# Performance work log

Hardware: AMD Instinct MI355X
Metric: run time of the kernel (lower is better)

The kernel has to match this reference:

```python
import jax, jax.numpy as jnp
import numpy as np

BATCH, NUM_M, NUM_USER, FEAT_B = 512, 64, 32, 62
CH = [64, 512, 512, 512]  # digital_channel; input = 2 (D feat) + 62 (B_norm feat)


def setup_inputs() -> dict:
    key = jax.random.key(0)
    ks = jax.random.split(key, 12)
    D = jax.random.normal(ks[0], (BATCH, NUM_USER, 2), dtype=jnp.float32)
    B = jax.random.uniform(ks[1], (BATCH, NUM_M, NUM_USER, FEAT_B), dtype=jnp.float32)
    P_pow_normalized = jnp.float32(1.0)
    D_0 = jax.random.normal(ks[2], (BATCH, NUM_USER, 2), dtype=jnp.float32)
    # MLP params: Lin(64,512)+ReLU, Lin(512,512)+ReLU, Lin(512,512)+ReLU, Lin(512,2)+Sigmoid
    def lin(k, fin, fout):
        bound = 1.0 / np.sqrt(fin)
        kw, kb = jax.random.split(k)
        W = jax.random.uniform(kw, (fin, fout), dtype=jnp.float32, minval=-bound, maxval=bound)
        b = jax.random.uniform(kb, (fout,), dtype=jnp.float32, minval=-bound, maxval=bound)
        return W, b
    W1, b1 = lin(ks[3], CH[0], CH[1])
    W2, b2 = lin(ks[4], CH[1], CH[2])
    W3, b3 = lin(ks[5], CH[2], CH[3])
    W4, b4 = lin(ks[6], CH[3], 2)
    return {"D": D, "B": B, "P_pow_normalized": P_pow_normalized, "D_0": D_0,
            "W1": W1, "b1": b1, "W2": W2, "b2": b2,
            "W3": W3, "b3": b3, "W4": W4, "b4": b4}


def reference(D, B, P_pow_normalized, D_0, W1, b1, W2, b2, W3, b3, W4, b4):
    # aggregate analog-side messages over antennas (dim 1): [batch, num_user, feat_B]
    B_norm = jnp.sum(B, axis=1)
    # per-user gather + concat -> [batch, num_user, ch0]
    x = jnp.concatenate([D, B_norm], axis=-1)
    # MLP applied row-wise (row ordering in the torch loop is irrelevant to the math)
    h = jax.nn.relu(x @ W1 + b1)
    h = jax.nn.relu(h @ W2 + b2)
    h = jax.nn.relu(h @ W3 + b3)
    D_1 = jax.nn.sigmoid(h @ W4 + b4)  # [batch, num_user, 2]
    # per-batch normalize over users, scale by power budget
    D_sum = jnp.sum(D_1, axis=1, keepdims=True)  # [batch, 1, 2]
    return P_pow_normalized * (D_1 / D_sum)
```

## Files before the change

### kernel.cpp

```cpp
#include <hip/hip_runtime.h>
#include <hip/hip_bf16.h>
#include <cstdint>
#include <cstddef>

#define BATCH 512
#define NUSER 32
#define NM    64
#define FEATB 62

typedef short bf16x8 __attribute__((ext_vector_type(8)));
typedef float f32x4  __attribute__((ext_vector_type(4)));
typedef float f32x4v __attribute__((ext_vector_type(4)));

__device__ __forceinline__ float bf2f(short s) {
    union { unsigned int u; float f; } v;
    v.u = ((unsigned int)(unsigned short)s) << 16;
    return v.f;
}

__global__ void transpose_cvt_all_kernel(
        const float* __restrict__ W1, const float* __restrict__ W2,
        const float* __restrict__ W3, const float* __restrict__ W4,
        __hip_bfloat16* __restrict__ WT1, __hip_bfloat16* __restrict__ WT2,
        __hip_bfloat16* __restrict__ WT3, __hip_bfloat16* __restrict__ WT4) {
    __shared__ float t[64][65];
    const int idx = blockIdx.x;
    const float* W; __hip_bfloat16* WT; int K, N, kt, nt;
    if (idx < 8)        { W = W1; WT = WT1; K = 64;  N = 512; kt = 0;             nt = idx;          }
    else if (idx < 72)  { W = W2; WT = WT2; K = 512; N = 512; kt = (idx-8) >> 3;  nt = (idx-8) & 7;  }
    else if (idx < 136) { W = W3; WT = WT3; K = 512; N = 512; kt = (idx-72) >> 3; nt = (idx-72) & 7; }
    else                { W = W4; WT = WT4; K = 512; N = 2;   kt = idx - 136;     nt = 0;            }
    const int k0 = kt * 64, n0 = nt * 64;
    #pragma unroll
    for (int i = 0; i < 16; ++i) {
        int lin = threadIdx.x + i * 256;
        int r = lin >> 6, c = lin & 63;
        if (k0 + r < K && n0 + c < N) t[r][c] = W[(size_t)(k0 + r) * N + (n0 + c)];
    }
    __syncthreads();
    #pragma unroll
    for (int i = 0; i < 16; ++i) {
        int lin = threadIdx.x + i * 256;
        int r = lin >> 6, c = lin & 63;
        if (n0 + r < N && k0 + c < K)
            WT[(size_t)(n0 + r) * K + (k0 + c)] = __float2bfloat16(t[c][r]);
    }
}

__device__ __forceinline__ void xs_store_pair(char* xs, int row, int col, float a, float b) {
    __hip_bfloat162 h;
    h.x = __float2bfloat16(a); h.y = __float2bfloat16(b);
    *reinterpret_cast<__hip_bfloat162*>(
        xs + (((unsigned)row * 128u + (unsigned)col * 2u) ^ ((unsigned)(row & 7) << 4))) = h;
}
__device__ __forceinline__ void xs_store4(char* xs, int j, float s0, float s1, float s2, float s3) {
    const int e = 4 * j;
    const int user = e / FEATB, feat = e % FEATB;
    xs_store_pair(xs, user, 2 + feat, s0, s1);
    if (feat == 60) xs_store_pair(xs, user + 1, 2, s2, s3);
    else            xs_store_pair(xs, user, 4 + feat, s2, s3);
}

template<int K, int ASTRIDE>
__device__ __forceinline__ void mlp_layer(const char* a_lds,
                                          const __hip_bfloat16* __restrict__ wt,
                                          const float* __restrict__ bias,
                                          char* out_lds,
                                          int wave, int lane) {
    f32x4 acc[2][8] = {};
    const int colbase = wave * 128;
    const int lrow = lane & 15;
    const int kg   = (lane >> 4) * 8;
    const unsigned int sw = (unsigned int)(lrow & 7) << 4;

    #pragma unroll 2
    for (int ks = 0; ks < K / 32; ++ks) {
        const int k0 = ks * 32 + kg;
        bf16x8 a0 = *reinterpret_cast<const bf16x8*>(a_lds + ((((unsigned)lrow        * ASTRIDE + k0 * 2)) ^ sw));
        bf16x8 a1 = *reinterpret_cast<const bf16x8*>(a_lds + ((((unsigned)(16 + lrow) * ASTRIDE + k0 * 2)) ^ sw));
        bf16x8 bfrag[8];
        #pragma unroll
        for (int n = 0; n < 8; ++n) {
            const int col = colbase + n * 16 + lrow;
            bfrag[n] = *reinterpret_cast<const bf16x8*>(wt + (size_t)col * K + k0);
        }
        #pragma unroll
        for (int n = 0; n < 8; ++n) {
            acc[0][n] = __builtin_amdgcn_mfma_f32_16x16x32_bf16(a0, bfrag[n], acc[0][n], 0, 0, 0);
            acc[1][n] = __builtin_amdgcn_mfma_f32_16x16x32_bf16(a1, bfrag[n], acc[1][n], 0, 0, 0);
        }
    }

    const int rg = (lane >> 4) * 4;
    #pragma unroll
    for (int m = 0; m < 2; ++m) {
        #pragma unroll
        for (int n = 0; n < 8; ++n) {
            const int col = colbase + n * 16 + lrow;
            const float bv = bias[col];
            #pragma unroll
            for (int r = 0; r < 4; ++r) {
                const int row = m * 16 + rg + r;
                float v = acc[m][n][r] + bv;
                v = fmaxf(v, 0.f);
                *reinterpret_cast<__hip_bfloat16*>(
                    out_lds + (((unsigned)row * 1024u + (unsigned)col * 2u) ^ ((unsigned)(row & 7) << 4)))
                    = __float2bfloat16(v);
            }
        }
    }
}

__global__ __launch_bounds__(256, 2) void fused_kernel(
    const float* __restrict__ B, const float* __restrict__ D,
    const __hip_bfloat16* __restrict__ WT1, const float* __restrict__ b1,
    const __hip_bfloat16* __restrict__ WT2, const float* __restrict__ b2,
    const __hip_bfloat16* __restrict__ WT3, const float* __restrict__ b3,
    const __hip_bfloat16* __restrict__ WT4, const float* __restrict__ b4,
    const float* __restrict__ Pp, float* __restrict__ out) {

    __shared__ __align__(16) char xs[NUSER * 64 * 2];
    __shared__ __align__(16) char act0[NUSER * 512 * 2];
    __shared__ __align__(16) char act1[NUSER * 512 * 2];
    __shared__ float d1s[NUSER][2];
    __shared__ float colsum[2];

    const int batch = blockIdx.x;
    const int tid = threadIdx.x;
    const int wave = tid >> 6, lane = tid & 63;

    {
        const f32x4v* p = reinterpret_cast<const f32x4v*>(B + (size_t)batch * (NM * NUSER * FEATB));
        const int j0 = tid, j1 = tid + 256;
        const bool hasj1 = (j1 < 496);
        f32x4v s0 = {0.f, 0.f, 0.f, 0.f};
        f32x4v s1 = {0.f, 0.f, 0.f, 0.f};
        #pragma unroll 4
        for (int m = 0; m < NM; ++m) {
            s0 += __builtin_nontemporal_load(p + (size_t)j0 + (size_t)m * 496);
            if (hasj1)
                s1 += __builtin_nontemporal_load(p + (size_t)j1 + (size_t)m * 496);
        }
        xs_store4(xs, j0, s0.x, s0.y, s0.z, s0.w);
        if (hasj1) {
            xs_store4(xs, j1, s1.x, s1.y, s1.z, s1.w);
        } else {
            const int dj = tid - 240;
            float4 v = reinterpret_cast<const float4*>(D + (size_t)batch * NUSER * 2)[dj];
            xs_store_pair(xs, 2 * dj,     0, v.x, v.y);
            xs_store_pair(xs, 2 * dj + 1, 0, v.z, v.w);
        }
    }
    __syncthreads();

    mlp_layer<64, 128>(xs, WT1, b1, act0, wave, lane);
    __syncthreads();
    mlp_layer<512, 1024>(act0, WT2, b2, act1, wave, lane);
    __syncthreads();
    mlp_layer<512, 1024>(act1, WT3, b3, act0, wave, lane);
    __syncthreads();

    {
        const int row = tid >> 3, col = (tid >> 2) & 1, part = tid & 3;
        float s = 0.f;
        #pragma unroll
        for (int kk = 0; kk < 128; kk += 8) {
            const int k = part * 128 + kk;
            bf16x8 av = *reinterpret_cast<const bf16x8*>(
                act0 + (((unsigned)row * 1024u + (unsigned)k * 2u) ^ ((unsigned)(row & 7) << 4)));
            bf16x8 wv = *reinterpret_cast<const bf16x8*>(WT4 + col * 512 + k);
            #pragma unroll
            for (int jj = 0; jj < 8; ++jj) s += bf2f(av[jj]) * bf2f(wv[jj]);
        }
        s += __shfl_xor(s, 1, 64);
        s += __shfl_xor(s, 2, 64);
        if (part == 0) {
            const float z = s + b4[col];
            d1s[row][col] = 1.f / (1.f + expf(-z));
        }
    }
    __syncthreads();

    if (tid < 2) {
        float s = 0.f;
        #pragma unroll
        for (int r = 0; r < NUSER; ++r) s += d1s[r][tid];
        colsum[tid] = s;
    }
    __syncthreads();
    if (tid < 64) {
        out[(size_t)batch * 64 + tid] = Pp[0] * d1s[tid >> 1][tid & 1] / colsum[tid & 1];
    }
}

extern "C" void kernel_launch(void* const* d_in, const int* in_sizes, int n_in,
                              void* d_out, int out_size, void* d_ws, size_t ws_size,
                              hipStream_t stream) {
    const float* D  = (const float*)d_in[0];
    const float* B  = (const float*)d_in[1];
    const float* Pp = (const float*)d_in[2];
    const float* W1 = (const float*)d_in[4];
    const float* b1 = (const float*)d_in[5];
    const float* W2 = (const float*)d_in[6];
    const float* b2 = (const float*)d_in[7];
    const float* W3 = (const float*)d_in[8];
    const float* b3 = (const float*)d_in[9];
    const float* W4 = (const float*)d_in[10];
    const float* b4 = (const float*)d_in[11];
    float* out = (float*)d_out;

    char* ws = (char*)d_ws;
    __hip_bfloat16* WT1 = (__hip_bfloat16*)(ws);
    __hip_bfloat16* WT2 = (__hip_bfloat16*)(ws + 65536);
    __hip_bfloat16* WT3 = (__hip_bfloat16*)(ws + 65536 + 524288);
    __hip_bfloat16* WT4 = (__hip_bfloat16*)(ws + 65536 + 524288 + 524288);

    transpose_cvt_all_kernel<<<144, 256, 0, stream>>>(W1, W2, W3, W4, WT1, WT2, WT3, WT4);

    fused_kernel<<<BATCH, 256, 0, stream>>>(B, D, WT1, b1, WT2, b2, WT3, b3,
                                            WT4, b4, Pp, out);
}
```

Baseline: 421.9 us.

## Process two batches per block with 512 threads and in-place activations

Each block now handles two batch items (64 rows), using 8 waves with a 64x64 MFMA tile per wave instead of 32x128. This doubles the M dimension per block, so each weight fragment loaded from global/L2 is reused across twice as many rows. A single activation buffer is updated in place, with an extra barrier before the writeback, to keep LDS use in check. The trade-offs are half as many blocks (256 across the CUs), an added sync per layer, and more accumulator registers per lane.

```diff
diff --git a/kernel.cpp b/kernel.cpp
--- a/kernel.cpp
+++ b/kernel.cpp
@@ -7,6 +7,8 @@
 #define NUSER 32
 #define NM    64
 #define FEATB 62
+
+#define SLICE_F4 (NM * NUSER * FEATB / 4)
 
 typedef short bf16x8 __attribute__((ext_vector_type(8)));
 typedef float f32x4  __attribute__((ext_vector_type(4)));
@@ -53,22 +55,23 @@
     *reinterpret_cast<__hip_bfloat162*>(
         xs + (((unsigned)row * 128u + (unsigned)col * 2u) ^ ((unsigned)(row & 7) << 4))) = h;
 }
-__device__ __forceinline__ void xs_store4(char* xs, int j, float s0, float s1, float s2, float s3) {
-    const int e = 4 * j;
-    const int user = e / FEATB, feat = e % FEATB;
+__device__ __forceinline__ void xs_store4(char* xs, int rowbase, int jj,
+                                          float s0, float s1, float s2, float s3) {
+    const int e = 4 * jj;
+    const int user = rowbase + e / FEATB, feat = e % FEATB;
     xs_store_pair(xs, user, 2 + feat, s0, s1);
     if (feat == 60) xs_store_pair(xs, user + 1, 2, s2, s3);
     else            xs_store_pair(xs, user, 4 + feat, s2, s3);
 }
 
-template<int K, int ASTRIDE>
+template<int K, int ASTRIDE, bool INPLACE>
 __device__ __forceinline__ void mlp_layer(const char* a_lds,
                                           const __hip_bfloat16* __restrict__ wt,
                                           const float* __restrict__ bias,
                                           char* out_lds,
                                           int wave, int lane) {
-    f32x4 acc[2][8] = {};
-    const int colbase = wave * 128;
+    f32x4 acc[4][4] = {};
+    const int colbase = wave * 64;
     const int lrow = lane & 15;
     const int kg   = (lane >> 4) * 8;
     const unsigned int sw = (unsigned int)(lrow & 7) << 4;
@@ -76,26 +79,31 @@
     #pragma unroll 2
     for (int ks = 0; ks < K / 32; ++ks) {
         const int k0 = ks * 32 + kg;
-        bf16x8 a0 = *reinterpret_cast<const bf16x8*>(a_lds + ((((unsigned)lrow        * ASTRIDE + k0 * 2)) ^ sw));
-        bf16x8 a1 = *reinterpret_cast<const bf16x8*>(a_lds + ((((unsigned)(16 + lrow) * ASTRIDE + k0 * 2)) ^ sw));
-        bf16x8 bfrag[8];
-        #pragma unroll
-        for (int n = 0; n < 8; ++n) {
+        bf16x8 a[4];
+        #pragma unroll
+        for (int m = 0; m < 4; ++m)
+            a[m] = *reinterpret_cast<const bf16x8*>(
+                a_lds + ((((unsigned)(m * 16 + lrow) * ASTRIDE + k0 * 2)) ^ sw));
+        bf16x8 bfrag[4];
+        #pragma unroll
+        for (int n = 0; n < 4; ++n) {
             const int col = colbase + n * 16 + lrow;
             bfrag[n] = *reinterpret_cast<const bf16x8*>(wt + (size_t)col * K + k0);
         }
         #pragma unroll
-        for (int n = 0; n < 8; ++n) {
-            acc[0][n] = __builtin_amdgcn_mfma_f32_16x16x32_bf16(a0, bfrag[n], acc[0][n], 0, 0, 0);
-            acc[1][n] = __builtin_amdgcn_mfma_f32_16x16x32_bf16(a1, bfrag[n], acc[1][n], 0, 0, 0);
-        }
-    }
+        for (int n = 0; n < 4; ++n)
+            #pragma unroll
+            for (int m = 0; m < 4; ++m)
+                acc[m][n] = __builtin_amdgcn_mfma_f32_16x16x32_bf16(a[m], bfrag[n], acc[m][n], 0, 0, 0);
+    }
+
+    if (INPLACE) __syncthreads();
 
     const int rg = (lane >> 4) * 4;
     #pragma unroll
-    for (int m = 0; m < 2; ++m) {
-        #pragma unroll
-        for (int n = 0; n < 8; ++n) {
+    for (int m = 0; m < 4; ++m) {
+        #pragma unroll
+        for (int n = 0; n < 4; ++n) {
             const int col = colbase + n * 16 + lrow;
             const float bv = bias[col];
             #pragma unroll
@@ -111,7 +119,7 @@
     }
 }
 
-__global__ __launch_bounds__(256, 2) void fused_kernel(
+__global__ __launch_bounds__(512, 2) void fused_kernel(
     const float* __restrict__ B, const float* __restrict__ D,
     const __hip_bfloat16* __restrict__ WT1, const float* __restrict__ b1,
     const __hip_bfloat16* __restrict__ WT2, const float* __restrict__ b2,
@@ -119,45 +127,51 @@
     const __hip_bfloat16* __restrict__ WT4, const float* __restrict__ b4,
     const float* __restrict__ Pp, float* __restrict__ out) {
 
-    __shared__ __align__(16) char xs[NUSER * 64 * 2];
-    __shared__ __align__(16) char act0[NUSER * 512 * 2];
-    __shared__ __align__(16) char act1[NUSER * 512 * 2];
-    __shared__ float d1s[NUSER][2];
-    __shared__ float colsum[2];
-
-    const int batch = blockIdx.x;
+    __shared__ __align__(16) char xs[64 * 64 * 2];
+    __shared__ __align__(16) char act[64 * 512 * 2];
+    __shared__ float d1s[64][2];
+    __shared__ float colsum[2][2];
+
+    const int b0 = blockIdx.x * 2;
     const int tid = threadIdx.x;
     const int wave = tid >> 6, lane = tid & 63;
 
     {
-        const f32x4v* p = reinterpret_cast<const f32x4v*>(B + (size_t)batch * (NM * NUSER * FEATB));
-        const int j0 = tid, j1 = tid + 256;
-        const bool hasj1 = (j1 < 496);
+        const f32x4v* p = reinterpret_cast<const f32x4v*>(B) + (size_t)b0 * SLICE_F4;
+        const bool s0_b1 = (tid >= 496);
+        const int  jj0   = s0_b1 ? tid - 496 : tid;
+        const bool has1  = (tid < 480);
+        const int  jj1   = tid + 16;
+        const f32x4v* p0 = p + (s0_b1 ? SLICE_F4 : 0) + jj0;
+        const f32x4v* p1 = p + SLICE_F4 + jj1;
         f32x4v s0 = {0.f, 0.f, 0.f, 0.f};
         f32x4v s1 = {0.f, 0.f, 0.f, 0.f};
-        #pragma unroll 4
+        #pragma unroll 8
         for (int m = 0; m < NM; ++m) {
-            s0 += __builtin_nontemporal_load(p + (size_t)j0 + (size_t)m * 496);
-            if (hasj1)
-                s1 += __builtin_nontemporal_load(p + (size_t)j1 + (size_t)m * 496);
-        }
-        xs_store4(xs, j0, s0.x, s0.y, s0.z, s0.w);
-        if (hasj1) {
-            xs_store4(xs, j1, s1.x, s1.y, s1.z, s1.w);
+            s0 += __builtin_nontemporal_load(p0 + (size_t)m * 496);
+            if (has1)
+                s1 += __builtin_nontemporal_load(p1 + (size_t)m * 496);
+        }
+        xs_store4(xs, s0_b1 ? 32 : 0, jj0, s0.x, s0.y, s0.z, s0.w);
+        if (has1) {
+            xs_store4(xs, 32, jj1, s1.x, s1.y, s1.z, s1.w);
         } else {
-            const int dj = tid - 240;
-            float4 v = reinterpret_cast<const float4*>(D + (size_t)batch * NUSER * 2)[dj];
-            xs_store_pair(xs, 2 * dj,     0, v.x, v.y);
-            xs_store_pair(xs, 2 * dj + 1, 0, v.z, v.w);
-        }
-    }
-    __syncthreads();
-
-    mlp_layer<64, 128>(xs, WT1, b1, act0, wave, lane);
-    __syncthreads();
-    mlp_layer<512, 1024>(act0, WT2, b2, act1, wave, lane);
-    __syncthreads();
-    mlp_layer<512, 1024>(act1, WT3, b3, act0, wave, lane);
+            const bool db1 = (tid >= 496);
+            const int  dj  = db1 ? tid - 496 : tid - 480;
+            const int  rb  = db1 ? 32 : 0;
+            float4 v = reinterpret_cast<const float4*>(
+                           D + (size_t)(b0 + (db1 ? 1 : 0)) * NUSER * 2)[dj];
+            xs_store_pair(xs, rb + 2 * dj,     0, v.x, v.y);
+            xs_store_pair(xs, rb + 2 * dj + 1, 0, v.z, v.w);
+        }
+    }
+    __syncthreads();
+
+    mlp_layer<64, 128, false>(xs, WT1, b1, act, wave, lane);
+    __syncthreads();
+    mlp_layer<512, 1024, true>(act, WT2, b2, act, wave, lane);
+    __syncthreads();
+    mlp_layer<512, 1024, true>(act, WT3, b3, act, wave, lane);
     __syncthreads();
 
     {
@@ -167,7 +181,7 @@
         for (int kk = 0; kk < 128; kk += 8) {
             const int k = part * 128 + kk;
             bf16x8 av = *reinterpret_cast<const bf16x8*>(
-                act0 + (((unsigned)row * 1024u + (unsigned)k * 2u) ^ ((unsigned)(row & 7) << 4)));
+                act + (((unsigned)row * 1024u + (unsigned)k * 2u) ^ ((unsigned)(row & 7) << 4)));
             bf16x8 wv = *reinterpret_cast<const bf16x8*>(WT4 + col * 512 + k);
             #pragma unroll
             for (int jj = 0; jj < 8; ++jj) s += bf2f(av[jj]) * bf2f(wv[jj]);
@@ -181,15 +195,18 @@
     }
     __syncthreads();
 
-    if (tid < 2) {
+    if (tid < 4) {
+        const int bb = tid >> 1, cc = tid & 1;
         float s = 0.f;
         #pragma unroll
-        for (int r = 0; r < NUSER; ++r) s += d1s[r][tid];
-        colsum[tid] = s;
-    }
-    __syncthreads();
-    if (tid < 64) {
-        out[(size_t)batch * 64 + tid] = Pp[0] * d1s[tid >> 1][tid & 1] / colsum[tid & 1];
+        for (int r = 0; r < NUSER; ++r) s += d1s[bb * 32 + r][cc];
+        colsum[bb][cc] = s;
+    }
+    __syncthreads();
+    if (tid < 128) {
+        const int bb = tid >> 6, idx = tid & 63;
+        out[(size_t)(b0 + bb) * 64 + idx] =
+            Pp[0] * d1s[bb * 32 + (idx >> 1)][idx & 1] / colsum[bb][idx & 1];
     }
 }
 
@@ -217,6 +234,6 @@
 
     transpose_cvt_all_kernel<<<144, 256, 0, stream>>>(W1, W2, W3, W4, WT1, WT2, WT3, WT4);
 
-    fused_kernel<<<BATCH, 256, 0, stream>>>(B, D, WT1, b1, WT2, b2, WT3, b3,
-                                            WT4, b4, Pp, out);
-}
+    fused_kernel<<<BATCH / 2, 512, 0, stream>>>(B, D, WT1, b1, WT2, b2, WT3, b3,
+                                                WT4, b4, Pp, out);
+}
```

Measured after the change: 397.4 us. 1.06x faster.
